# Kernel tuning notes

Hardware: AMD Instinct MI355X
Metric: run time of the kernel (lower is better)

## Reference

```python
import jax, jax.numpy as jnp
import numpy as np

# Human3.6M skeleton: 16 bones over 17 joints
SKELETON = [(0,1),(1,2),(2,3),(0,4),(4,5),(5,6),(0,7),(7,8),(8,9),(9,10),(8,11),(11,12),(12,13),(8,14),(14,15),(15,16)]
PARENT = jnp.array([p for p, c in SKELETON], dtype=jnp.int32)
CHILD = jnp.array([c for p, c in SKELETON], dtype=jnp.int32)
NUM_BONES = 16
EPS = 1e-9


def setup_inputs() -> dict:
    key = jax.random.key(0)
    k1, k2, k3, k4, k5 = jax.random.split(key, 5)
    B, J = 1000000, 17
    pred_jts = jax.random.normal(k1, (B, J, 3), dtype=jnp.float32)
    gt_bl = jax.random.uniform(k2, (B, NUM_BONES), dtype=jnp.float32)
    anchor_scores = jax.random.uniform(k3, (B, J), dtype=jnp.float32)
    # ShiftAttention params: fc1 (32->16), fc2 (16->32), no bias; stored as [in, out]
    W1 = jax.random.normal(k4, (2 * NUM_BONES, NUM_BONES), dtype=jnp.float32) * (2.0 / (2 * NUM_BONES)) ** 0.5
    W2 = jax.random.normal(k5, (NUM_BONES, 2 * NUM_BONES), dtype=jnp.float32) * (2.0 / NUM_BONES) ** 0.5
    return {"pred_jts": pred_jts, "gt_bl": gt_bl, "anchor_scores": anchor_scores, "W1": W1, "W2": W2}


def reference(pred_jts, gt_bl, anchor_scores, W1, W2):
    B = pred_jts.shape[0]
    # per-edge gather: bone vectors [B, 16, 3]
    diff = pred_jts[:, PARENT, :] - pred_jts[:, CHILD, :]
    bl_norm = jnp.linalg.norm(diff, axis=-1)            # [B, 16]
    dis_bl = gt_bl - bl_norm                            # bone-length error
    a_p = anchor_scores[:, PARENT]
    a_c = anchor_scores[:, CHILD]
    a_sum = a_p + a_c + EPS
    # split correction between parent (weighted by child score) and child
    move_bl = jnp.stack([dis_bl * a_c / a_sum, dis_bl * a_p / a_sum], axis=-1)  # [B, 16, 2]
    # ShiftAttention gate: sigmoid(relu(x W1) W2)
    x = move_bl.reshape(B, 2 * NUM_BONES)
    gate = jax.nn.sigmoid(jax.nn.relu(x @ W1) @ W2).reshape(B, NUM_BONES, 2)
    move_bl = move_bl * gate
    # unit bone directions and per-edge forces
    unit = diff / (bl_norm[..., None] + EPS)            # [B, 16, 3]
    force_parent = move_bl[..., 0:1] * unit
    force_child = -move_bl[..., 1:2] * unit
    # scatter-add forces into joints (duplicate joint indices accumulate)
    move_jts = jnp.zeros_like(pred_jts).at[:, PARENT].add(force_parent).at[:, CHILD].add(force_child)
    return pred_jts + move_jts
```

## Files before the change

kernel.cpp:

```cpp
#include <hip/hip_runtime.h>

#define DEV __device__ __forceinline__

#define LDS_FENCE() asm volatile("s_waitcnt lgkmcnt(0)" ::: "memory")
#define VM_FENCE()  asm volatile("s_waitcnt vmcnt(0)" ::: "memory")

typedef __fp16 h16x2 __attribute__((ext_vector_type(2)));

DEV void gload_lds16(const void* g, void* lds) {
    __builtin_amdgcn_global_load_lds(
        (const __attribute__((address_space(1))) void*)g,
        (__attribute__((address_space(3))) void*)lds,
        16, 0, 0);
}

DEV float dot2(h16x2 a, h16x2 b, float acc) {
    asm("v_dot2_f32_f16 %0, %1, %2, %0" : "+v"(acc) : "v"(a), "v"(b));
    return acc;
}

DEV h16x2 f2h(float a, float b) { return __builtin_amdgcn_cvt_pkrtz(a, b); }

DEV float fast_sigmoid(float v) {
    return __builtin_amdgcn_rcpf(1.0f + __builtin_amdgcn_exp2f(-1.4426950408889634f * v));
}

DEV void compute_sample(const float (&p)[51], const float (&a)[17], const float (&g)[16],
                        const float4* sW1h4, const float4* sW2h4, float (&o)[51])
{
    constexpr int PAR[16] = {0,1,2,0,4,5,0,7,8,9,8,11,12,8,14,15};
    constexpr int CHI[16] = {1,2,3,4,5,6,7,8,9,10,11,12,13,14,15,16};

    float x[32], invn[16];
    #pragma unroll
    for (int k = 0; k < 16; ++k) {
        const int P = PAR[k] * 3, C = CHI[k] * 3;
        const float dx = p[P]   - p[C];
        const float dy = p[P+1] - p[C+1];
        const float dz = p[P+2] - p[C+2];
        const float n  = __builtin_amdgcn_sqrtf(fmaf(dx,dx, fmaf(dy,dy, dz*dz)));
        const float dis = g[k] - n;
        const float ap = a[PAR[k]], ac = a[CHI[k]];
        const float inv_asum = __builtin_amdgcn_rcpf(ap + ac + 1e-9f);
        x[2*k]   = dis * ac * inv_asum;
        x[2*k+1] = dis * ap * inv_asum;
        invn[k]  = __builtin_amdgcn_rcpf(n + 1e-9f);
    }

    h16x2 xp[16];
    #pragma unroll
    for (int ip = 0; ip < 16; ++ip) xp[ip] = f2h(x[2*ip], x[2*ip+1]);

    float y[16];
    #pragma unroll
    for (int j = 0; j < 16; ++j) y[j] = 0.f;
    #pragma unroll
    for (int ip = 0; ip < 16; ++ip) {
        #pragma unroll
        for (int jj = 0; jj < 4; ++jj) {
            const float4 wq = sW1h4[ip*4 + jj];
            y[4*jj+0] = dot2(xp[ip], __builtin_bit_cast(h16x2, wq.x), y[4*jj+0]);
            y[4*jj+1] = dot2(xp[ip], __builtin_bit_cast(h16x2, wq.y), y[4*jj+1]);
            y[4*jj+2] = dot2(xp[ip], __builtin_bit_cast(h16x2, wq.z), y[4*jj+2]);
            y[4*jj+3] = dot2(xp[ip], __builtin_bit_cast(h16x2, wq.w), y[4*jj+3]);
        }
    }
    h16x2 hp[8];
    #pragma unroll
    for (int jp = 0; jp < 8; ++jp)
        hp[jp] = f2h(fmaxf(y[2*jp], 0.f), fmaxf(y[2*jp+1], 0.f));

    float gg[32];
    #pragma unroll
    for (int c = 0; c < 32; ++c) gg[c] = 0.f;
    #pragma unroll
    for (int jp = 0; jp < 8; ++jp) {
        #pragma unroll
        for (int cc = 0; cc < 8; ++cc) {
            const float4 wq = sW2h4[jp*8 + cc];
            gg[4*cc+0] = dot2(hp[jp], __builtin_bit_cast(h16x2, wq.x), gg[4*cc+0]);
            gg[4*cc+1] = dot2(hp[jp], __builtin_bit_cast(h16x2, wq.y), gg[4*cc+1]);
            gg[4*cc+2] = dot2(hp[jp], __builtin_bit_cast(h16x2, wq.z), gg[4*cc+2]);
            gg[4*cc+3] = dot2(hp[jp], __builtin_bit_cast(h16x2, wq.w), gg[4*cc+3]);
        }
    }

    float xg[32];
    #pragma unroll
    for (int c = 0; c < 32; ++c) xg[c] = x[c] * fast_sigmoid(gg[c]);
    #pragma unroll
    for (int k = 0; k < 16; ++k) {
        xg[2*k]   *= invn[k];
        xg[2*k+1] *= invn[k];
    }

    #pragma unroll
    for (int j = 0; j < 17; ++j) {
        float ox = p[3*j], oy = p[3*j+1], oz = p[3*j+2];
        #pragma unroll
        for (int k = 0; k < 16; ++k) {
            if (PAR[k] == j || CHI[k] == j) {
                const int P = PAR[k] * 3, C = CHI[k] * 3;
                const float dx = p[P]   - p[C];
                const float dy = p[P+1] - p[C+1];
                const float dz = p[P+2] - p[C+2];
                const float s = (PAR[k] == j) ? xg[2*k] : -xg[2*k+1];
                ox = fmaf(s, dx, ox);
                oy = fmaf(s, dy, oy);
                oz = fmaf(s, dz, oz);
            }
        }
        o[3*j]   = ox;
        o[3*j+1] = oy;
        o[3*j+2] = oz;
    }
}

__global__ __launch_bounds__(256, 2) void projts_kernel(
    const float* __restrict__ pred,
    const float* __restrict__ gt,
    const float* __restrict__ anc,
    const float* __restrict__ gW1,
    const float* __restrict__ gW2,
    float* __restrict__ out,
    int B)
{
    constexpr int ROW = 51;
    constexpr int WBUF = 64 * ROW;
    constexpr int ABUF = 64 * 17;

    __shared__ h16x2 sW1h[256] __attribute__((aligned(16)));
    __shared__ h16x2 sW2h[256] __attribute__((aligned(16)));
    __shared__ float sbuf[4][WBUF] __attribute__((aligned(16)));
    __shared__ float abuf[4][ABUF] __attribute__((aligned(16)));

    const int t = threadIdx.x;

    {
        const int ip = t >> 4, j = t & 15;
        sW1h[t] = f2h(gW1[32*ip + j], gW1[32*ip + 16 + j]);
        const int jp = t >> 5, c = t & 31;
        sW2h[t] = f2h(gW2[64*jp + c], gW2[64*jp + 32 + c]);
    }
    __syncthreads();

    const float4* sW1h4 = reinterpret_cast<const float4*>(sW1h);
    const float4* sW2h4 = reinterpret_cast<const float4*>(sW2h);

    const int w = t >> 6;
    const int l = t & 63;
    const long long wavebase = ((long long)blockIdx.x * 4 + w) * 64;
    if (wavebase >= B) return;

    float* buf  = sbuf[w];
    float4* buf4 = reinterpret_cast<float4*>(buf);
    float* abf  = abuf[w];

    if (wavebase + 64 <= (long long)B) {
        float p[51], a[17], o[51];

        const char* srcB = reinterpret_cast<const char*>(pred + (size_t)wavebase * ROW);
        const char* ascB = reinterpret_cast<const char*>(anc + (size_t)wavebase * 17);
        char* bufB = reinterpret_cast<char*>(buf);
        char* abfB = reinterpret_cast<char*>(abf);

        #pragma unroll
        for (int i = 0; i < 12; ++i)
            gload_lds16(srcB + (size_t)(i*64 + l)*16, bufB + i*1024);
        if (l < 48)
            gload_lds16(srcB + (size_t)(768 + l)*16, bufB + 12*1024);

        #pragma unroll
        for (int i = 0; i < 4; ++i)
            gload_lds16(ascB + (size_t)(i*64 + l)*16, abfB + i*1024);
        if (l < 16)
            gload_lds16(ascB + (size_t)(256 + l)*16, abfB + 4*1024);

        const float4* gsrc4 = reinterpret_cast<const float4*>(gt + (size_t)(wavebase + l) * 16);
        const float4 gq0 = gsrc4[0], gq1 = gsrc4[1], gq2 = gsrc4[2], gq3 = gsrc4[3];

        VM_FENCE();

        #pragma unroll
        for (int j = 0; j < ROW; ++j) p[j] = buf[l*ROW + j];
        #pragma unroll
        for (int j = 0; j < 17; ++j) a[j] = abf[l*17 + j];
        LDS_FENCE();

        const float g[16] = {gq0.x,gq0.y,gq0.z,gq0.w, gq1.x,gq1.y,gq1.z,gq1.w,
                             gq2.x,gq2.y,gq2.z,gq2.w, gq3.x,gq3.y,gq3.z,gq3.w};

        compute_sample(p, a, g, sW1h4, sW2h4, o);

        #pragma unroll
        for (int j = 0; j < ROW; ++j) buf[l*ROW + j] = o[j];
        LDS_FENCE();

        float4* dst4 = reinterpret_cast<float4*>(out + (size_t)wavebase * ROW);
        #pragma unroll
        for (int i = 0; i < 12; ++i) dst4[i*64 + l] = buf4[i*64 + l];
        if (l < 48) dst4[768 + l] = buf4[768 + l];
    } else {
        const long long b = wavebase + l;
        if (b < B) {
            float p[51], a[17], g[16], o[51];
            const float* pj = pred + (size_t)b * 51;
            #pragma unroll
            for (int j = 0; j < 51; ++j) p[j] = pj[j];
            const float* ab = anc + (size_t)b * 17;
            #pragma unroll
            for (int j = 0; j < 17; ++j) a[j] = ab[j];
            const float* gb = gt + (size_t)b * 16;
            #pragma unroll
            for (int j = 0; j < 16; ++j) g[j] = gb[j];

            compute_sample(p, a, g, sW1h4, sW2h4, o);

            float* ob = out + (size_t)b * 51;
            #pragma unroll
            for (int j = 0; j < 51; ++j) ob[j] = o[j];
        }
    }
}

extern "C" void kernel_launch(void* const* d_in, const int* in_sizes, int n_in,
                              void* d_out, int out_size, void* d_ws, size_t ws_size,
                              hipStream_t stream) {
    const float* pred = (const float*)d_in[0];
    const float* gt   = (const float*)d_in[1];
    const float* anc  = (const float*)d_in[2];
    const float* W1   = (const float*)d_in[3];
    const float* W2   = (const float*)d_in[4];
    float* out = (float*)d_out;

    const int B = in_sizes[0] / 51;
    const int blocks = (B + 255) / 256;
    hipLaunchKernelGGL(projts_kernel, dim3(blocks), dim3(256), 0, stream,
                       pred, gt, anc, W1, W2, out, B);
}
```

Before: 109.5 us.

## Drop anchor LDS buffer and stage anchors through reused pose buffer for occupancy

The dedicated per-wave anchor LDS buffer is removed. Anchor scores are now loaded into registers with vector loads, written into the per-wave pose LDS buffer once the pose values have been read out, and then read back transposed per lane. This cuts per-block LDS enough that three blocks can fit on a CU, and launch bounds are raised to 3 to match. Scheduling barriers are added to the wait fences so the compiler cannot move memory ops across them. The tighter register budget at three blocks per CU risks spills, and the extra LDS round trip adds serialization.

```diff
diff --git a/kernel.cpp b/kernel.cpp
--- a/kernel.cpp
+++ b/kernel.cpp
@@ -2,8 +2,10 @@
 
 #define DEV __device__ __forceinline__
 
-#define LDS_FENCE() asm volatile("s_waitcnt lgkmcnt(0)" ::: "memory")
-#define VM_FENCE()  asm volatile("s_waitcnt vmcnt(0)" ::: "memory")
+#define LDS_FENCE() do { asm volatile("s_waitcnt lgkmcnt(0)" ::: "memory"); \
+                         __builtin_amdgcn_sched_barrier(0); } while (0)
+#define VM_FENCE()  do { asm volatile("s_waitcnt vmcnt(0)" ::: "memory");  \
+                         __builtin_amdgcn_sched_barrier(0); } while (0)
 
 typedef __fp16 h16x2 __attribute__((ext_vector_type(2)));
 
@@ -116,7 +118,7 @@
     }
 }
 
-__global__ __launch_bounds__(256, 2) void projts_kernel(
+__global__ __launch_bounds__(256, 3) void projts_kernel(
     const float* __restrict__ pred,
     const float* __restrict__ gt,
     const float* __restrict__ anc,
@@ -127,12 +129,10 @@
 {
     constexpr int ROW = 51;
     constexpr int WBUF = 64 * ROW;
-    constexpr int ABUF = 64 * 17;
 
     __shared__ h16x2 sW1h[256] __attribute__((aligned(16)));
     __shared__ h16x2 sW2h[256] __attribute__((aligned(16)));
     __shared__ float sbuf[4][WBUF] __attribute__((aligned(16)));
-    __shared__ float abuf[4][ABUF] __attribute__((aligned(16)));
 
     const int t = threadIdx.x;
 
@@ -154,15 +154,12 @@
 
     float* buf  = sbuf[w];
     float4* buf4 = reinterpret_cast<float4*>(buf);
-    float* abf  = abuf[w];
 
     if (wavebase + 64 <= (long long)B) {
         float p[51], a[17], o[51];
 
         const char* srcB = reinterpret_cast<const char*>(pred + (size_t)wavebase * ROW);
-        const char* ascB = reinterpret_cast<const char*>(anc + (size_t)wavebase * 17);
         char* bufB = reinterpret_cast<char*>(buf);
-        char* abfB = reinterpret_cast<char*>(abf);
 
         #pragma unroll
         for (int i = 0; i < 12; ++i)
@@ -170,11 +167,12 @@
         if (l < 48)
             gload_lds16(srcB + (size_t)(768 + l)*16, bufB + 12*1024);
 
-        #pragma unroll
-        for (int i = 0; i < 4; ++i)
-            gload_lds16(ascB + (size_t)(i*64 + l)*16, abfB + i*1024);
-        if (l < 16)
-            gload_lds16(ascB + (size_t)(256 + l)*16, abfB + 4*1024);
+        const float4* asrc4 = reinterpret_cast<const float4*>(anc + (size_t)wavebase * 17);
+        float4 ar0 = asrc4[0*64 + l];
+        float4 ar1 = asrc4[1*64 + l];
+        float4 ar2 = asrc4[2*64 + l];
+        float4 ar3 = asrc4[3*64 + l];
+        float4 ar4 = asrc4[256 + (l & 15)];
 
         const float4* gsrc4 = reinterpret_cast<const float4*>(gt + (size_t)(wavebase + l) * 16);
         const float4 gq0 = gsrc4[0], gq1 = gsrc4[1], gq2 = gsrc4[2], gq3 = gsrc4[3];
@@ -183,8 +181,17 @@
 
         #pragma unroll
         for (int j = 0; j < ROW; ++j) p[j] = buf[l*ROW + j];
-        #pragma unroll
-        for (int j = 0; j < 17; ++j) a[j] = abf[l*17 + j];
+        LDS_FENCE();
+
+        buf4[0*64 + l] = ar0;
+        buf4[1*64 + l] = ar1;
+        buf4[2*64 + l] = ar2;
+        buf4[3*64 + l] = ar3;
+        buf4[256 + l]  = ar4;
+        LDS_FENCE();
+
+        #pragma unroll
+        for (int j = 0; j < 17; ++j) a[j] = buf[l*17 + j];
         LDS_FENCE();
 
         const float g[16] = {gq0.x,gq0.y,gq0.z,gq0.w, gq1.x,gq1.y,gq1.z,gq1.w,
```

Result: slower. 214.3 us (+95.7%).
